# Optimization experiments

Measured on AMD Instinct MI355X. Metric: run time of the kernel, lower is better.

## Reference

```python
import jax, jax.numpy as jnp
import numpy as np

B, IN, H = 256, 256, 512


def setup_inputs() -> dict:
    key = jax.random.key(0)
    ks = jax.random.split(key, 16)
    s = 0.02  # weight init scale
    d = {
        "x": jax.random.normal(ks[0], (B, IN), jnp.float32),
        "C_prev": jax.random.normal(ks[1], (B, H, H), jnp.float32) * 0.1,
        "n_prev": jax.random.normal(ks[2], (B, H), jnp.float32) * 0.1,
    }
    for j, nm in enumerate(["q", "k", "v", "i", "f", "o"]):
        d["W" + nm] = jax.random.normal(ks[3 + 2 * j], (H, IN), jnp.float32) * s
        d["b" + nm] = jnp.zeros((H,), jnp.float32)
    return d


def reference(x, C_prev, n_prev, Wq, bq, Wk, bk, Wv, bv, Wi, bi, Wf, bf, Wo, bo):
    # x: [B, In]; C_prev: [B, H, H]; n_prev: [B, H]
    h = Wq.shape[0]
    inv_sqrt_h = 1.0 / jnp.sqrt(jnp.asarray(h, x.dtype))
    q = x @ Wq.T + bq                              # [B, H]
    k = (x @ Wk.T + bk) * inv_sqrt_h               # [B, H] (scaled key)
    v = x @ Wv.T + bv                              # [B, H]
    i = jnp.exp(x @ Wi.T + bi)                     # exponential input gate
    f = jax.nn.sigmoid(x @ Wf.T + bf)              # forget gate
    o = jax.nn.sigmoid(x @ Wo.T + bo)              # output gate
    # Gates broadcast over the LAST axis of the [H, H] matrix state,
    # matching f * C_prev / i * jnp.outer(v, k) in the original.
    C_t = f[:, None, :] * C_prev + i[:, None, :] * (v[:, :, None] * k[:, None, :])  # [B, H, H]
    n_t = f * n_prev + i * k                       # [B, H]
    denom = jnp.maximum(jnp.abs(jnp.einsum("bh,bh->b", n_t, q)), 1.0)  # [B]
    h_t = o * (jnp.einsum("bij,bj->bi", C_t, q) / denom[:, None])      # [B, H]
    return (C_t, n_t, h_t)
```

## Files before the change

### kernel.cpp

```cpp
#include <hip/hip_runtime.h>
#include <math.h>

#define BATCH 256
#define INDIM 256
#define HDIM  512
#define BH    (BATCH * HDIM)

__device__ __forceinline__ float sigmoidf_(float v) {
    return 1.0f / (1.0f + expf(-v));
}

__global__ __launch_bounds__(256) void gates_kernel(
    const float* __restrict__ x,
    const float* __restrict__ Wq, const float* __restrict__ bq,
    const float* __restrict__ Wk, const float* __restrict__ bk,
    const float* __restrict__ Wv, const float* __restrict__ bv,
    const float* __restrict__ Wi, const float* __restrict__ bi,
    const float* __restrict__ Wf, const float* __restrict__ bf,
    const float* __restrict__ Wo, const float* __restrict__ bo,
    float* __restrict__ gates)
{
    __shared__ float Wt[64][65];
    __shared__ float Xt[64][65];

    const int m0 = blockIdx.x * 64;
    const int n0 = blockIdx.y * 64;
    const int t  = threadIdx.x;

    const int g  = m0 >> 9;
    const int h0 = m0 & 511;

    const float* W; const float* bias;
    switch (g) {
        case 0: W = Wq; bias = bq; break;
        case 1: W = Wk; bias = bk; break;
        case 2: W = Wv; bias = bv; break;
        case 3: W = Wi; bias = bi; break;
        case 4: W = Wf; bias = bf; break;
        default: W = Wo; bias = bo; break;
    }
    const float* Wg = W + (size_t)h0 * INDIM;

    const int tx = t & 15;
    const int ty = t >> 4;

    float acc[4][4] = {};

    for (int k0 = 0; k0 < INDIM; k0 += 64) {
        const int kk4 = (t & 15) * 4;
        const int row = t >> 4;
        #pragma unroll
        for (int rr = 0; rr < 4; rr++) {
            const int mr = row + rr * 16;
            const float4 w = *(const float4*)(Wg + mr * INDIM + k0 + kk4);
            Wt[mr][kk4 + 0] = w.x; Wt[mr][kk4 + 1] = w.y;
            Wt[mr][kk4 + 2] = w.z; Wt[mr][kk4 + 3] = w.w;
            const float4 xv = *(const float4*)(x + (n0 + mr) * INDIM + k0 + kk4);
            Xt[mr][kk4 + 0] = xv.x; Xt[mr][kk4 + 1] = xv.y;
            Xt[mr][kk4 + 2] = xv.z; Xt[mr][kk4 + 3] = xv.w;
        }
        __syncthreads();
        #pragma unroll 8
        for (int kk = 0; kk < 64; kk++) {
            float a[4], bb[4];
            #pragma unroll
            for (int i2 = 0; i2 < 4; i2++) a[i2] = Wt[ty * 4 + i2][kk];
            #pragma unroll
            for (int j = 0; j < 4; j++) bb[j] = Xt[tx * 4 + j][kk];
            #pragma unroll
            for (int i2 = 0; i2 < 4; i2++)
                #pragma unroll
                for (int j = 0; j < 4; j++)
                    acc[i2][j] += a[i2] * bb[j];
        }
        __syncthreads();
    }

    const float inv_sqrt_h = 0.044194173824159216f;
    #pragma unroll
    for (int i2 = 0; i2 < 4; i2++) {
        const int h = h0 + ty * 4 + i2;
        const float bv_ = bias[h];
        #pragma unroll
        for (int j = 0; j < 4; j++) {
            const int n = n0 + tx * 4 + j;
            float val = acc[i2][j] + bv_;
            if (g == 1)      val *= inv_sqrt_h;
            else if (g == 3) val = expf(val);
            else if (g >= 4) val = sigmoidf_(val);
            gates[(size_t)g * BH + (size_t)n * HDIM + h] = val;
        }
    }
}

__global__ __launch_bounds__(256) void nt_denom_kernel(
    const float* __restrict__ gates,
    const float* __restrict__ n_prev,
    float* __restrict__ n_out,
    float* __restrict__ denom)
{
    const int b = blockIdx.x;
    const int t = threadIdx.x;
    const int lane = t & 63;
    const int wave = t >> 6;

    const float* qb = gates + 0 * (size_t)BH + (size_t)b * HDIM;
    const float* kb = gates + 1 * (size_t)BH + (size_t)b * HDIM;
    const float* ib = gates + 3 * (size_t)BH + (size_t)b * HDIM;
    const float* fb = gates + 4 * (size_t)BH + (size_t)b * HDIM;
    const float* npv = n_prev + (size_t)b * HDIM;

    float partial = 0.0f;
    for (int h = t; h < HDIM; h += 256) {
        const float nt = fb[h] * npv[h] + ib[h] * kb[h];
        n_out[(size_t)b * HDIM + h] = nt;
        partial += nt * qb[h];
    }
    #pragma unroll
    for (int off = 32; off > 0; off >>= 1)
        partial += __shfl_down(partial, off);

    __shared__ float red[4];
    if (lane == 0) red[wave] = partial;
    __syncthreads();
    if (t == 0) {
        const float s = red[0] + red[1] + red[2] + red[3];
        denom[b] = fmaxf(fabsf(s), 1.0f);
    }
}

__global__ __launch_bounds__(256) void cell_kernel(
    const float* __restrict__ C_prev,
    const float* __restrict__ gates,
    const float* __restrict__ denom_arr,
    float* __restrict__ C_out,
    float* __restrict__ h_out)
{
    const int blk    = blockIdx.x;
    const int b      = blk >> 4;
    const int rchunk = blk & 15;
    const int wave   = threadIdx.x >> 6;
    const int lane   = threadIdx.x & 63;

    const float* qb = gates + 0 * (size_t)BH + (size_t)b * HDIM;
    const float* kb = gates + 1 * (size_t)BH + (size_t)b * HDIM;
    const float* vb = gates + 2 * (size_t)BH + (size_t)b * HDIM;
    const float* ib = gates + 3 * (size_t)BH + (size_t)b * HDIM;
    const float* fb = gates + 4 * (size_t)BH + (size_t)b * HDIM;
    const float* ob = gates + 5 * (size_t)BH + (size_t)b * HDIM;

    const int c0 = lane * 4;

    const float4 f0 = *(const float4*)(fb + c0);
    const float4 f1 = *(const float4*)(fb + 256 + c0);
    const float4 q0 = *(const float4*)(qb + c0);
    const float4 q1 = *(const float4*)(qb + 256 + c0);
    const float4 i0 = *(const float4*)(ib + c0);
    const float4 i1 = *(const float4*)(ib + 256 + c0);
    const float4 k0 = *(const float4*)(kb + c0);
    const float4 k1 = *(const float4*)(kb + 256 + c0);
    float4 a0, a1;
    a0.x = i0.x * k0.x; a0.y = i0.y * k0.y; a0.z = i0.z * k0.z; a0.w = i0.w * k0.w;
    a1.x = i1.x * k1.x; a1.y = i1.y * k1.y; a1.z = i1.z * k1.z; a1.w = i1.w * k1.w;

    const float dinv = 1.0f / denom_arr[b];

    const size_t base = (size_t)b * HDIM * HDIM;
    const int r0 = rchunk * 32 + wave * 8;

    #pragma unroll
    for (int rr = 0; rr < 8; rr++) {
        const int r = r0 + rr;
        const float vr = vb[r];
        const float* cp = C_prev + base + (size_t)r * HDIM;
        float*       co = C_out  + base + (size_t)r * HDIM;

        const float4 c0v = *(const float4*)(cp + c0);
        const float4 c1v = *(const float4*)(cp + 256 + c0);

        float4 t0, t1;
        t0.x = f0.x * c0v.x + vr * a0.x;
        t0.y = f0.y * c0v.y + vr * a0.y;
        t0.z = f0.z * c0v.z + vr * a0.z;
        t0.w = f0.w * c0v.w + vr * a0.w;
        t1.x = f1.x * c1v.x + vr * a1.x;
        t1.y = f1.y * c1v.y + vr * a1.y;
        t1.z = f1.z * c1v.z + vr * a1.z;
        t1.w = f1.w * c1v.w + vr * a1.w;

        *(float4*)(co + c0)       = t0;
        *(float4*)(co + 256 + c0) = t1;

        float dot = t0.x * q0.x + t0.y * q0.y + t0.z * q0.z + t0.w * q0.w
                  + t1.x * q1.x + t1.y * q1.y + t1.z * q1.z + t1.w * q1.w;
        #pragma unroll
        for (int off = 32; off > 0; off >>= 1)
            dot += __shfl_down(dot, off);

        if (lane == 0)
            h_out[(size_t)b * HDIM + r] = ob[r] * dot * dinv;
    }
}

extern "C" void kernel_launch(void* const* d_in, const int* in_sizes, int n_in,
                              void* d_out, int out_size, void* d_ws, size_t ws_size,
                              hipStream_t stream) {
    const float* x      = (const float*)d_in[0];
    const float* C_prev = (const float*)d_in[1];
    const float* n_prev = (const float*)d_in[2];
    const float* Wq = (const float*)d_in[3];  const float* bq = (const float*)d_in[4];
    const float* Wk = (const float*)d_in[5];  const float* bk = (const float*)d_in[6];
    const float* Wv = (const float*)d_in[7];  const float* bv = (const float*)d_in[8];
    const float* Wi = (const float*)d_in[9];  const float* bi = (const float*)d_in[10];
    const float* Wf = (const float*)d_in[11]; const float* bf = (const float*)d_in[12];
    const float* Wo = (const float*)d_in[13]; const float* bo = (const float*)d_in[14];

    float* out   = (float*)d_out;
    float* C_out = out;
    float* n_out = out + (size_t)BATCH * HDIM * HDIM;
    float* h_out = n_out + (size_t)BATCH * HDIM;

    float* gates = (float*)d_ws;
    float* denom = gates + 6 * (size_t)BH;

    dim3 gridA(3072 / 64, BATCH / 64);
    gates_kernel<<<gridA, 256, 0, stream>>>(x, Wq, bq, Wk, bk, Wv, bv,
                                            Wi, bi, Wf, bf, Wo, bo, gates);
    nt_denom_kernel<<<BATCH, 256, 0, stream>>>(gates, n_prev, n_out, denom);
    cell_kernel<<<BATCH * (HDIM / 32), 256, 0, stream>>>(C_prev, gates, denom,
                                                         C_out, h_out);
}
```

Baseline: 491.6 us.

## Fuse n_t/denominator into cell kernel, vectorize gate stores, nontemporal C streaming

Removes the separate n_t/denominator kernel by having each cell block recompute n_t and the q-dot reduction for its batch row, with only the first row chunk writing n_out. The gates GEMM swaps operand roles so each thread writes a contiguous float4 along the hidden dimension instead of strided scalars. The cell loop batches four rows of C_prev loads before compute and uses nontemporal loads and stores for the large streaming state. The trade-off is redundant n_t work across 16 blocks per batch plus an extra block barrier.

```diff
diff --git a/kernel.cpp b/kernel.cpp
--- a/kernel.cpp
+++ b/kernel.cpp
@@ -5,6 +5,8 @@
 #define INDIM 256
 #define HDIM  512
 #define BH    (BATCH * HDIM)
+
+typedef float f32x4 __attribute__((ext_vector_type(4)));
 
 __device__ __forceinline__ float sigmoidf_(float v) {
     return 1.0f / (1.0f + expf(-v));
@@ -64,9 +66,9 @@
         for (int kk = 0; kk < 64; kk++) {
             float a[4], bb[4];
             #pragma unroll
-            for (int i2 = 0; i2 < 4; i2++) a[i2] = Wt[ty * 4 + i2][kk];
-            #pragma unroll
-            for (int j = 0; j < 4; j++) bb[j] = Xt[tx * 4 + j][kk];
+            for (int i2 = 0; i2 < 4; i2++) a[i2] = Xt[ty * 4 + i2][kk];
+            #pragma unroll
+            for (int j = 0; j < 4; j++) bb[j] = Wt[tx * 4 + j][kk];
             #pragma unroll
             for (int i2 = 0; i2 < 4; i2++)
                 #pragma unroll
@@ -77,70 +79,45 @@
     }
 
     const float inv_sqrt_h = 0.044194173824159216f;
+    const int hb = h0 + tx * 4;
+    const float4 b4 = *(const float4*)(bias + hb);
+
     #pragma unroll
     for (int i2 = 0; i2 < 4; i2++) {
-        const int h = h0 + ty * 4 + i2;
-        const float bv_ = bias[h];
-        #pragma unroll
-        for (int j = 0; j < 4; j++) {
-            const int n = n0 + tx * 4 + j;
-            float val = acc[i2][j] + bv_;
-            if (g == 1)      val *= inv_sqrt_h;
-            else if (g == 3) val = expf(val);
-            else if (g >= 4) val = sigmoidf_(val);
-            gates[(size_t)g * BH + (size_t)n * HDIM + h] = val;
-        }
-    }
-}
-
-__global__ __launch_bounds__(256) void nt_denom_kernel(
+        const int n = n0 + ty * 4 + i2;
+        float4 r;
+        r.x = acc[i2][0] + b4.x;
+        r.y = acc[i2][1] + b4.y;
+        r.z = acc[i2][2] + b4.z;
+        r.w = acc[i2][3] + b4.w;
+        if (g == 1) {
+            r.x *= inv_sqrt_h; r.y *= inv_sqrt_h;
+            r.z *= inv_sqrt_h; r.w *= inv_sqrt_h;
+        } else if (g == 3) {
+            r.x = expf(r.x); r.y = expf(r.y);
+            r.z = expf(r.z); r.w = expf(r.w);
+        } else if (g >= 4) {
+            r.x = sigmoidf_(r.x); r.y = sigmoidf_(r.y);
+            r.z = sigmoidf_(r.z); r.w = sigmoidf_(r.w);
+        }
+        *(float4*)(gates + (size_t)g * BH + (size_t)n * HDIM + hb) = r;
+    }
+}
+
+__global__ __launch_bounds__(256) void cell_kernel(
+    const float* __restrict__ C_prev,
     const float* __restrict__ gates,
     const float* __restrict__ n_prev,
     float* __restrict__ n_out,
-    float* __restrict__ denom)
-{
-    const int b = blockIdx.x;
-    const int t = threadIdx.x;
-    const int lane = t & 63;
-    const int wave = t >> 6;
-
-    const float* qb = gates + 0 * (size_t)BH + (size_t)b * HDIM;
-    const float* kb = gates + 1 * (size_t)BH + (size_t)b * HDIM;
-    const float* ib = gates + 3 * (size_t)BH + (size_t)b * HDIM;
-    const float* fb = gates + 4 * (size_t)BH + (size_t)b * HDIM;
-    const float* npv = n_prev + (size_t)b * HDIM;
-
-    float partial = 0.0f;
-    for (int h = t; h < HDIM; h += 256) {
-        const float nt = fb[h] * npv[h] + ib[h] * kb[h];
-        n_out[(size_t)b * HDIM + h] = nt;
-        partial += nt * qb[h];
-    }
-    #pragma unroll
-    for (int off = 32; off > 0; off >>= 1)
-        partial += __shfl_down(partial, off);
-
-    __shared__ float red[4];
-    if (lane == 0) red[wave] = partial;
-    __syncthreads();
-    if (t == 0) {
-        const float s = red[0] + red[1] + red[2] + red[3];
-        denom[b] = fmaxf(fabsf(s), 1.0f);
-    }
-}
-
-__global__ __launch_bounds__(256) void cell_kernel(
-    const float* __restrict__ C_prev,
-    const float* __restrict__ gates,
-    const float* __restrict__ denom_arr,
     float* __restrict__ C_out,
     float* __restrict__ h_out)
 {
     const int blk    = blockIdx.x;
     const int b      = blk >> 4;
     const int rchunk = blk & 15;
-    const int wave   = threadIdx.x >> 6;
-    const int lane   = threadIdx.x & 63;
+    const int t      = threadIdx.x;
+    const int wave   = t >> 6;
+    const int lane   = t & 63;
 
     const float* qb = gates + 0 * (size_t)BH + (size_t)b * HDIM;
     const float* kb = gates + 1 * (size_t)BH + (size_t)b * HDIM;
@@ -148,6 +125,7 @@
     const float* ib = gates + 3 * (size_t)BH + (size_t)b * HDIM;
     const float* fb = gates + 4 * (size_t)BH + (size_t)b * HDIM;
     const float* ob = gates + 5 * (size_t)BH + (size_t)b * HDIM;
+    const float* npv = n_prev + (size_t)b * HDIM;
 
     const int c0 = lane * 4;
 
@@ -159,46 +137,79 @@
     const float4 i1 = *(const float4*)(ib + 256 + c0);
     const float4 k0 = *(const float4*)(kb + c0);
     const float4 k1 = *(const float4*)(kb + 256 + c0);
+
+    const float nt0 = fb[t] * npv[t] + ib[t] * kb[t];
+    const float nt1 = fb[t + 256] * npv[t + 256] + ib[t + 256] * kb[t + 256];
+    if (rchunk == 0) {
+        n_out[(size_t)b * HDIM + t]       = nt0;
+        n_out[(size_t)b * HDIM + t + 256] = nt1;
+    }
+    float p = nt0 * qb[t] + nt1 * qb[t + 256];
+    #pragma unroll
+    for (int off = 32; off > 0; off >>= 1)
+        p += __shfl_down(p, off);
+
+    __shared__ float red[4];
+    __shared__ float dsh;
+    if (lane == 0) red[wave] = p;
+    __syncthreads();
+    if (t == 0)
+        dsh = 1.0f / fmaxf(fabsf(red[0] + red[1] + red[2] + red[3]), 1.0f);
+    __syncthreads();
+    const float dinv = dsh;
+
     float4 a0, a1;
     a0.x = i0.x * k0.x; a0.y = i0.y * k0.y; a0.z = i0.z * k0.z; a0.w = i0.w * k0.w;
     a1.x = i1.x * k1.x; a1.y = i1.y * k1.y; a1.z = i1.z * k1.z; a1.w = i1.w * k1.w;
 
-    const float dinv = 1.0f / denom_arr[b];
-
     const size_t base = (size_t)b * HDIM * HDIM;
     const int r0 = rchunk * 32 + wave * 8;
 
     #pragma unroll
-    for (int rr = 0; rr < 8; rr++) {
-        const int r = r0 + rr;
-        const float vr = vb[r];
-        const float* cp = C_prev + base + (size_t)r * HDIM;
-        float*       co = C_out  + base + (size_t)r * HDIM;
-
-        const float4 c0v = *(const float4*)(cp + c0);
-        const float4 c1v = *(const float4*)(cp + 256 + c0);
-
-        float4 t0, t1;
-        t0.x = f0.x * c0v.x + vr * a0.x;
-        t0.y = f0.y * c0v.y + vr * a0.y;
-        t0.z = f0.z * c0v.z + vr * a0.z;
-        t0.w = f0.w * c0v.w + vr * a0.w;
-        t1.x = f1.x * c1v.x + vr * a1.x;
-        t1.y = f1.y * c1v.y + vr * a1.y;
-        t1.z = f1.z * c1v.z + vr * a1.z;
-        t1.w = f1.w * c1v.w + vr * a1.w;
-
-        *(float4*)(co + c0)       = t0;
-        *(float4*)(co + 256 + c0) = t1;
-
-        float dot = t0.x * q0.x + t0.y * q0.y + t0.z * q0.z + t0.w * q0.w
-                  + t1.x * q1.x + t1.y * q1.y + t1.z * q1.z + t1.w * q1.w;
-        #pragma unroll
-        for (int off = 32; off > 0; off >>= 1)
-            dot += __shfl_down(dot, off);
-
-        if (lane == 0)
-            h_out[(size_t)b * HDIM + r] = ob[r] * dot * dinv;
+    for (int grp = 0; grp < 2; grp++) {
+        const int rb = r0 + grp * 4;
+
+        f32x4 cA[4], cB[4];
+        #pragma unroll
+        for (int rr = 0; rr < 4; rr++) {
+            const float* cp = C_prev + base + (size_t)(rb + rr) * HDIM;
+            cA[rr] = __builtin_nontemporal_load((const f32x4*)(cp + c0));
+            cB[rr] = __builtin_nontemporal_load((const f32x4*)(cp + 256 + c0));
+        }
+
+        float dots[4];
+        #pragma unroll
+        for (int rr = 0; rr < 4; rr++) {
+            const int r = rb + rr;
+            const float vr = vb[r];
+
+            f32x4 t0, t1;
+            t0.x = f0.x * cA[rr].x + vr * a0.x;
+            t0.y = f0.y * cA[rr].y + vr * a0.y;
+            t0.z = f0.z * cA[rr].z + vr * a0.z;
+            t0.w = f0.w * cA[rr].w + vr * a0.w;
+            t1.x = f1.x * cB[rr].x + vr * a1.x;
+            t1.y = f1.y * cB[rr].y + vr * a1.y;
+            t1.z = f1.z * cB[rr].z + vr * a1.z;
+            t1.w = f1.w * cB[rr].w + vr * a1.w;
+
+            float* co = C_out + base + (size_t)r * HDIM;
+            __builtin_nontemporal_store(t0, (f32x4*)(co + c0));
+            __builtin_nontemporal_store(t1, (f32x4*)(co + 256 + c0));
+
+            dots[rr] = t0.x * q0.x + t0.y * q0.y + t0.z * q0.z + t0.w * q0.w
+                     + t1.x * q1.x + t1.y * q1.y + t1.z * q1.z + t1.w * q1.w;
+        }
+
+        #pragma unroll
+        for (int rr = 0; rr < 4; rr++) {
+            float d = dots[rr];
+            #pragma unroll
+            for (int off = 32; off > 0; off >>= 1)
+                d += __shfl_down(d, off);
+            if (lane == 0)
+                h_out[(size_t)b * HDIM + rb + rr] = ob[rb + rr] * d * dinv;
+        }
     }
 }
 
@@ -221,12 +232,10 @@
     float* h_out = n_out + (size_t)BATCH * HDIM;
 
     float* gates = (float*)d_ws;
-    float* denom = gates + 6 * (size_t)BH;
 
     dim3 gridA(3072 / 64, BATCH / 64);
     gates_kernel<<<gridA, 256, 0, stream>>>(x, Wq, bq, Wk, bk, Wv, bv,
                                             Wi, bi, Wf, bf, Wo, bo, gates);
-    nt_denom_kernel<<<BATCH, 256, 0, stream>>>(gates, n_prev, n_out, denom);
-    cell_kernel<<<BATCH * (HDIM / 32), 256, 0, stream>>>(C_prev, gates, denom,
-                                                         C_out, h_out);
-}
+    cell_kernel<<<BATCH * (HDIM / 32), 256, 0, stream>>>(C_prev, gates, n_prev,
+                                                         n_out, C_out, h_out);
+}
```

Result: faster. 474.4 us (-3.5%).
